# Performance work log

Hardware: AMD Instinct MI355X
Metric: run time of the kernel (lower is better)

## Reference

```python
import jax, jax.numpy as jnp
import numpy as np

N_NODES = 50000
N_EDGES = 800000
N_GRAPHS = 64
IN_DIM = 128
HID = 64      # per-head channels of conv1
HEADS1 = 4
OUT_DIM = 128
NEG_SLOPE = 0.2


def setup_inputs() -> dict:
    key = jax.random.key(0)
    ks = jax.random.split(key, 12)
    x = jax.random.normal(ks[0], (N_NODES, IN_DIM), dtype=jnp.float32)
    src = jax.random.randint(ks[1], (N_EDGES,), 0, N_NODES, dtype=jnp.int32)
    dst = jax.random.randint(ks[2], (N_EDGES,), 0, N_NODES, dtype=jnp.int32)
    batch = jnp.sort(jax.random.randint(ks[3], (N_NODES,), 0, N_GRAPHS, dtype=jnp.int32))
    s = 0.1
    W1 = jax.random.normal(ks[4], (IN_DIM, HEADS1 * HID), dtype=jnp.float32) * s
    a_src1 = jax.random.normal(ks[5], (HEADS1, HID), dtype=jnp.float32) * s
    a_dst1 = jax.random.normal(ks[6], (HEADS1, HID), dtype=jnp.float32) * s
    b1 = jnp.zeros((HEADS1 * HID,), dtype=jnp.float32)
    W2 = jax.random.normal(ks[7], (HEADS1 * HID, OUT_DIM), dtype=jnp.float32) * s
    a_src2 = jax.random.normal(ks[8], (1, OUT_DIM), dtype=jnp.float32) * s
    a_dst2 = jax.random.normal(ks[9], (1, OUT_DIM), dtype=jnp.float32) * s
    b2 = jnp.zeros((OUT_DIM,), dtype=jnp.float32)
    return {"x": x, "src": src, "dst": dst, "batch": batch,
            "W1": W1, "a_src1": a_src1, "a_dst1": a_dst1, "b1": b1,
            "W2": W2, "a_src2": a_src2, "a_dst2": a_dst2, "b2": b2}


def gat_conv(x, src, dst, W, a_src, a_dst, b, heads, ch, concat):
    """PyG-style GATConv (self-loops already appended to src/dst)."""
    n = x.shape[0]
    h = (x @ W).reshape(n, heads, ch)                     # [N,H,C]
    al_s = jnp.einsum('nhc,hc->nh', h, a_src)             # per-node src score
    al_d = jnp.einsum('nhc,hc->nh', h, a_dst)             # per-node dst score
    e = jax.nn.leaky_relu(al_s[src] + al_d[dst], NEG_SLOPE)  # [E,H]
    # segment softmax over incoming edges of each dst node
    m = jax.ops.segment_max(e, dst, num_segments=n)
    ex = jnp.exp(e - m[dst])
    den = jax.ops.segment_sum(ex, dst, num_segments=n)
    alpha = ex / den[dst]                                 # [E,H]
    out = jax.ops.segment_sum(alpha[:, :, None] * h[src], dst, num_segments=n)  # [N,H,C]
    out = out.reshape(n, heads * ch) if concat else out.mean(axis=1)
    return out + b


def reference(x, src, dst, batch, W1, a_src1, a_dst1, b1, W2, a_src2, a_dst2, b2):
    n = x.shape[0]
    loop = jnp.arange(n, dtype=src.dtype)
    s = jnp.concatenate([src, loop])   # add_self_loops=True (PyG default)
    d = jnp.concatenate([dst, loop])
    h = jax.nn.relu(gat_conv(x, s, d, W1, a_src1, a_dst1, b1, HEADS1, HID, True))
    h = gat_conv(h, s, d, W2, a_src2, a_dst2, b2, 1, OUT_DIM, False)
    # global_mean_pool over graph ids
    sums = jax.ops.segment_sum(h, batch, num_segments=N_GRAPHS)
    cnts = jax.ops.segment_sum(jnp.ones((n,), h.dtype), batch, num_segments=N_GRAPHS)
    return sums / jnp.maximum(cnts, 1.0)[:, None]
```

## Files before the change

kernel.cpp:

```cpp
#include <hip/hip_runtime.h>
#include <math.h>

#define NN 50000
#define NE 800000
#define ETOT (NE + NN)
#define NG 64
#define IND 128
#define HID1 64
#define H1HEADS 4
#define D1 256
#define D2 128
#define NEG 0.2f
#define CAP 64

typedef __attribute__((ext_vector_type(8))) short bf16x8;
typedef __attribute__((ext_vector_type(4))) float f32x4;

__device__ __forceinline__ unsigned short bf16rne(float f) {
    unsigned u = __float_as_uint(f);
    u = (u + 0x7FFFu + ((u >> 16) & 1u)) >> 16;
    return (unsigned short)u;
}
__device__ __forceinline__ float bf2f(unsigned short u) {
    return __uint_as_float(((unsigned)u) << 16);
}
__device__ __forceinline__ bf16x8 pack8(float4 a, float4 b) {
    bf16x8 r;
    r[0] = (short)bf16rne(a.x); r[1] = (short)bf16rne(a.y);
    r[2] = (short)bf16rne(a.z); r[3] = (short)bf16rne(a.w);
    r[4] = (short)bf16rne(b.x); r[5] = (short)bf16rne(b.y);
    r[6] = (short)bf16rne(b.z); r[7] = (short)bf16rne(b.w);
    return r;
}

__global__ __launch_bounds__(256) void build_fill(
        const int* __restrict__ src, const int* __restrict__ dst,
        const float* __restrict__ W1, unsigned short* __restrict__ W1t,
        const float* __restrict__ W2, unsigned short* __restrict__ W2t,
        const int* __restrict__ batch,
        int* __restrict__ deg, int* __restrict__ csrF,
        int* __restrict__ gstart) {
    const long E0 = ETOT;
    const long E1 = E0 + (long)IND * D1;
    const long E2 = E1 + (long)D1 * D2;
    const long T  = E2 + NG + 1;
    long i = (long)blockIdx.x * 256 + threadIdx.x;
    if (i >= T) return;
    if (i < E0) {
        int s = (i < NE) ? src[i] : (int)(i - NE);
        int d = (i < NE) ? dst[i] : (int)(i - NE);
        int slot = atomicAdd(&deg[d], 1);
        if (slot < CAP) csrF[d * CAP + slot] = s;
    } else if (i < E1) {
        int j = (int)(i - E0);
        int c_ = j / IND, r_ = j % IND;
        W1t[j] = bf16rne(W1[(long)r_ * D1 + c_]);
    } else if (i < E2) {
        int j = (int)(i - E1);
        int c_ = j / D1, r_ = j % D1;
        W2t[j] = bf16rne(W2[(long)r_ * D2 + c_]);
    } else {
        int g = (int)(i - E2);
        if (g == NG) gstart[NG] = NN;
        else {
            int lo = 0, hi = NN;
            while (lo < hi) {
                int mid = (lo + hi) >> 1;
                if (batch[mid] < g) lo = mid + 1; else hi = mid;
            }
            gstart[g] = lo;
        }
    }
}

template<int K, int N, int H, int AF32>
__global__ __launch_bounds__(256) void mfma_gemm_sc(int M,
                                                    const void* __restrict__ Ap,
                                                    const unsigned short* __restrict__ Bt,
                                                    const float* __restrict__ a_s,
                                                    const float* __restrict__ a_d,
                                                    unsigned short* __restrict__ C,
                                                    float* __restrict__ al_s,
                                                    float* __restrict__ al_d) {
    constexpr int NT = N / 16;
    constexpr int FPH = NT / H;
    const int w = threadIdx.x >> 6, l = threadIdx.x & 63;
    const int brow = blockIdx.x * 128 + w * 32;
    const int lr = l & 15, lk = (l >> 4) * 8;
    const int ar0 = min(brow + lr, M - 1);
    const int ar1 = min(brow + 16 + lr, M - 1);
    f32x4 acc[2][NT] = {};
    #pragma unroll
    for (int k0 = 0; k0 < K; k0 += 32) {
        bf16x8 af0, af1;
        if constexpr (AF32) {
            const float* a0 = (const float*)Ap + (long)ar0 * K + lk + k0;
            const float* a1 = (const float*)Ap + (long)ar1 * K + lk + k0;
            af0 = pack8(*reinterpret_cast<const float4*>(a0),
                        *reinterpret_cast<const float4*>(a0 + 4));
            af1 = pack8(*reinterpret_cast<const float4*>(a1),
                        *reinterpret_cast<const float4*>(a1 + 4));
        } else {
            af0 = *reinterpret_cast<const bf16x8*>((const unsigned short*)Ap + (long)ar0 * K + lk + k0);
            af1 = *reinterpret_cast<const bf16x8*>((const unsigned short*)Ap + (long)ar1 * K + lk + k0);
        }
        #pragma unroll
        for (int n = 0; n < NT; ++n) {
            bf16x8 bv = *reinterpret_cast<const bf16x8*>(Bt + (long)(n * 16 + lr) * K + lk + k0);
            acc[0][n] = __builtin_amdgcn_mfma_f32_16x16x32_bf16(af0, bv, acc[0][n], 0, 0, 0);
            acc[1][n] = __builtin_amdgcn_mfma_f32_16x16x32_bf16(af1, bv, acc[1][n], 0, 0, 0);
        }
    }
    float asv[NT], adv[NT];
    #pragma unroll
    for (int n = 0; n < NT; ++n) { asv[n] = a_s[n * 16 + lr]; adv[n] = a_d[n * 16 + lr]; }
    #pragma unroll
    for (int g = 0; g < 2; ++g) {
        const int orow = brow + g * 16 + (l >> 4) * 4;
        #pragma unroll
        for (int j = 0; j < 4; ++j) {
            int r = orow + j;
            bool ok = r < M;
            #pragma unroll
            for (int n = 0; n < NT; ++n)
                if (ok) C[(long)r * N + n * 16 + lr] = bf16rne(acc[g][n][j]);
            #pragma unroll
            for (int h = 0; h < H; ++h) {
                float ss = 0.f, sd = 0.f;
                #pragma unroll
                for (int f = 0; f < FPH; ++f) {
                    int n = h * FPH + f;
                    ss += acc[g][n][j] * asv[n];
                    sd += acc[g][n][j] * adv[n];
                }
                #pragma unroll
                for (int o = 8; o > 0; o >>= 1) {
                    ss += __shfl_xor(ss, o);
                    sd += __shfl_xor(sd, o);
                }
                if (ok && lr == 0) {
                    al_s[(long)r * H + h] = ss;
                    al_d[(long)r * H + h] = sd;
                }
            }
        }
    }
}

template<int H, int C, int RELU, int OUTBF>
__global__ __launch_bounds__(256) void gat_gather(const int* __restrict__ deg,
                                                  const int* __restrict__ csrF,
                                                  const float* __restrict__ als,
                                                  const float* __restrict__ ald,
                                                  const unsigned short* __restrict__ Hb,
                                                  const float* __restrict__ bias,
                                                  void* __restrict__ outp_) {
    constexpr int D = H * C;
    constexpr int VPL = D / 64;
    constexpr int HP = (H == 4) ? 5 : 1;
    __shared__ float sW[4][64][HP];
    __shared__ int   sS[4][64];
    const int lane = threadIdx.x & 63;
    const int w = threadIdx.x >> 6;
    const int n = blockIdx.x * 4 + w;
    if (n >= NN) return;
    const int h = (lane * VPL) / C;

    float aldv[H];
    #pragma unroll
    for (int hh = 0; hh < H; ++hh) aldv[hh] = ald[(long)n * H + hh];

    float acc[VPL] = {};
    float den = 0.f;

    const int cnt = min(deg[n], CAP);
    const bool valid = lane < cnt;
    const int s_l = valid ? csrF[n * CAP + lane] : 0;
    if constexpr (H == 4) {
        float4 a4 = *reinterpret_cast<const float4*>(als + (long)s_l * 4);
        float xs[4] = {a4.x, a4.y, a4.z, a4.w};
        #pragma unroll
        for (int hh = 0; hh < 4; ++hh) {
            float x = xs[hh] + aldv[hh];
            x = (x >= 0.f) ? x : NEG * x;
            sW[w][lane][hh] = valid ? __expf(x) : 0.f;
        }
    } else {
        float x = als[s_l] + aldv[0];
        x = (x >= 0.f) ? x : NEG * x;
        sW[w][lane][0] = valid ? __expf(x) : 0.f;
    }
    sS[w][lane] = s_l;

    int j0 = 0;
    for (; j0 + 8 <= cnt; j0 += 8) {
        int se[8]; float we[8];
        #pragma unroll
        for (int t = 0; t < 8; ++t) {
            se[t] = sS[w][j0 + t];
            we[t] = sW[w][j0 + t][h];
        }
        #pragma unroll
        for (int t = 0; t < 8; ++t) den += we[t];
        if constexpr (VPL == 4) {
            ushort4 aa[8];
            #pragma unroll
            for (int t = 0; t < 8; ++t)
                aa[t] = *reinterpret_cast<const ushort4*>(Hb + (long)se[t] * D + lane * 4);
            #pragma unroll
            for (int t = 0; t < 8; ++t) {
                acc[0] += we[t] * bf2f(aa[t].x); acc[1] += we[t] * bf2f(aa[t].y);
                acc[2] += we[t] * bf2f(aa[t].z); acc[3] += we[t] * bf2f(aa[t].w);
            }
        } else {
            ushort2 aa[8];
            #pragma unroll
            for (int t = 0; t < 8; ++t)
                aa[t] = *reinterpret_cast<const ushort2*>(Hb + (long)se[t] * D + lane * 2);
            #pragma unroll
            for (int t = 0; t < 8; ++t) {
                acc[0] += we[t] * bf2f(aa[t].x); acc[1] += we[t] * bf2f(aa[t].y);
            }
        }
    }
    for (; j0 < cnt; j0 += 4) {
        int se[4]; float we[4];
        #pragma unroll
        for (int t = 0; t < 4; ++t) {
            se[t] = sS[w][j0 + t];
            we[t] = sW[w][j0 + t][h];
        }
        #pragma unroll
        for (int t = 0; t < 4; ++t) den += we[t];
        if constexpr (VPL == 4) {
            ushort4 aa[4];
            #pragma unroll
            for (int t = 0; t < 4; ++t)
                aa[t] = *reinterpret_cast<const ushort4*>(Hb + (long)se[t] * D + lane * 4);
            #pragma unroll
            for (int t = 0; t < 4; ++t) {
                acc[0] += we[t] * bf2f(aa[t].x); acc[1] += we[t] * bf2f(aa[t].y);
                acc[2] += we[t] * bf2f(aa[t].z); acc[3] += we[t] * bf2f(aa[t].w);
            }
        } else {
            ushort2 aa[4];
            #pragma unroll
            for (int t = 0; t < 4; ++t)
                aa[t] = *reinterpret_cast<const ushort2*>(Hb + (long)se[t] * D + lane * 2);
            #pragma unroll
            for (int t = 0; t < 4; ++t) {
                acc[0] += we[t] * bf2f(aa[t].x); acc[1] += we[t] * bf2f(aa[t].y);
            }
        }
    }

    float inv = 1.f / den;
    float v[VPL];
    #pragma unroll
    for (int k = 0; k < VPL; ++k) {
        v[k] = acc[k] * inv + bias[lane * VPL + k];
        if (RELU) v[k] = fmaxf(v[k], 0.f);
    }
    if constexpr (OUTBF) {
        unsigned short* o = (unsigned short*)outp_;
        if constexpr (VPL == 4) {
            ushort4 p; p.x = bf16rne(v[0]); p.y = bf16rne(v[1]);
            p.z = bf16rne(v[2]); p.w = bf16rne(v[3]);
            *reinterpret_cast<ushort4*>(o + (long)n * D + lane * 4) = p;
        } else {
            ushort2 p; p.x = bf16rne(v[0]); p.y = bf16rne(v[1]);
            *reinterpret_cast<ushort2*>(o + (long)n * D + lane * 2) = p;
        }
    } else {
        float* o = (float*)outp_;
        if constexpr (VPL == 4) {
            float4 p = {v[0], v[1], v[2], v[3]};
            *reinterpret_cast<float4*>(o + (long)n * D + lane * 4) = p;
        } else {
            float2 p = {v[0], v[1]};
            *reinterpret_cast<float2*>(o + (long)n * D + lane * 2) = p;
        }
    }
}

__global__ __launch_bounds__(256) void pool_graph(const unsigned short* __restrict__ out2b,
                                                  const int* __restrict__ gstart,
                                                  float* __restrict__ out) {
    __shared__ float2 part[4][64];
    const int g = blockIdx.x;
    const int ch2 = threadIdx.x & 63;
    const int q = threadIdx.x >> 6;
    const int s = gstart[g], e = gstart[g + 1];
    float2 acc = {0.f, 0.f};
    for (int r = s + q; r < e; r += 4) {
        ushort2 v = *reinterpret_cast<const ushort2*>(out2b + (long)r * D2 + ch2 * 2);
        acc.x += bf2f(v.x);
        acc.y += bf2f(v.y);
    }
    part[q][ch2] = acc;
    __syncthreads();
    if (q == 0) {
        float inv = 1.f / fmaxf((float)(e - s), 1.f);
        float2 v;
        v.x = (part[0][ch2].x + part[1][ch2].x + part[2][ch2].x + part[3][ch2].x) * inv;
        v.y = (part[0][ch2].y + part[1][ch2].y + part[2][ch2].y + part[3][ch2].y) * inv;
        *reinterpret_cast<float2*>(out + g * D2 + ch2 * 2) = v;
    }
}

extern "C" void kernel_launch(void* const* d_in, const int* in_sizes, int n_in,
                              void* d_out, int out_size, void* d_ws, size_t ws_size,
                              hipStream_t stream) {
    const float* x      = (const float*)d_in[0];
    const int*   src    = (const int*)d_in[1];
    const int*   dst    = (const int*)d_in[2];
    const int*   batch  = (const int*)d_in[3];
    const float* W1     = (const float*)d_in[4];
    const float* a_src1 = (const float*)d_in[5];
    const float* a_dst1 = (const float*)d_in[6];
    const float* b1     = (const float*)d_in[7];
    const float* W2     = (const float*)d_in[8];
    const float* a_src2 = (const float*)d_in[9];
    const float* a_dst2 = (const float*)d_in[10];
    const float* b2     = (const float*)d_in[11];
    float* out = (float*)d_out;

    float* ws   = (float*)d_ws;
    float* als1 = ws;
    float* ald1 = als1 + (long)NN * H1HEADS;
    float* als2 = als1;
    float* ald2 = als1 + NN;
    unsigned short* Hb1   = (unsigned short*)(ald1 + (long)NN * H1HEADS);
    unsigned short* out1b = Hb1 + (long)NN * D1;
    unsigned short* Hb2   = out1b + (long)NN * D1;
    unsigned short* out2b = Hb2 + (long)NN * D2;
    unsigned short* W1t   = out2b + (long)NN * D2;
    unsigned short* W2t   = W1t + D1 * IND;
    int* deg    = (int*)(W2t + D2 * D1);
    int* csrF   = deg + NN;
    int* gstart = csrF + (long)NN * CAP;

    (void)hipMemsetAsync(deg, 0, NN * sizeof(int), stream);
    {
        long total = (long)ETOT + IND * D1 + D1 * D2 + NG + 1;
        build_fill<<<(int)((total + 255) / 256), 256, 0, stream>>>(
            src, dst, W1, W1t, W2, W2t, batch, deg, csrF, gstart);
    }

    mfma_gemm_sc<IND, D1, H1HEADS, 1><<<(NN + 127) / 128, 256, 0, stream>>>(
        NN, x, W1t, a_src1, a_dst1, Hb1, als1, ald1);
    gat_gather<H1HEADS, HID1, 1, 1><<<(NN + 3) / 4, 256, 0, stream>>>(
        deg, csrF, als1, ald1, Hb1, b1, out1b);

    mfma_gemm_sc<D1, D2, 1, 0><<<(NN + 127) / 128, 256, 0, stream>>>(
        NN, out1b, W2t, a_src2, a_dst2, Hb2, als2, ald2);
    gat_gather<1, D2, 0, 1><<<(NN + 3) / 4, 256, 0, stream>>>(
        deg, csrF, als2, ald2, Hb2, b2, out2b);

    pool_graph<<<NG, 256, 0, stream>>>(out2b, gstart, out);
}
```

Before: 272.6 us.

## Split layer-1 gather into two half-feature passes over column halves

The layer-1 gather, which handled all 256 features per node in one wave, is split into two launches. Each launch handles 128 columns, i.e. two heads. Each pass touches only half of every source row, so the working set of the random gathers is smaller and more likely to stay in cache. In exchange, the CSR lists and attention scores are read twice, the weights are recomputed, and there is an extra launch. The layer-2 gather is specialised into its own non-template kernel with equivalent logic.

```diff
diff --git a/kernel.cpp b/kernel.cpp
--- a/kernel.cpp
+++ b/kernel.cpp
@@ -147,50 +147,41 @@
     }
 }
 
-template<int H, int C, int RELU, int OUTBF>
-__global__ __launch_bounds__(256) void gat_gather(const int* __restrict__ deg,
-                                                  const int* __restrict__ csrF,
-                                                  const float* __restrict__ als,
-                                                  const float* __restrict__ ald,
-                                                  const unsigned short* __restrict__ Hb,
-                                                  const float* __restrict__ bias,
-                                                  void* __restrict__ outp_) {
-    constexpr int D = H * C;
-    constexpr int VPL = D / 64;
-    constexpr int HP = (H == 4) ? 5 : 1;
-    __shared__ float sW[4][64][HP];
+template<int P>
+__global__ __launch_bounds__(256) void gather1_half(const int* __restrict__ deg,
+                                                    const int* __restrict__ csrF,
+                                                    const float* __restrict__ als,
+                                                    const float* __restrict__ ald,
+                                                    const unsigned short* __restrict__ Hb,
+                                                    const float* __restrict__ bias,
+                                                    unsigned short* __restrict__ outp) {
+    __shared__ float sW[4][64][2];
     __shared__ int   sS[4][64];
     const int lane = threadIdx.x & 63;
     const int w = threadIdx.x >> 6;
     const int n = blockIdx.x * 4 + w;
     if (n >= NN) return;
-    const int h = (lane * VPL) / C;
-
-    float aldv[H];
-    #pragma unroll
-    for (int hh = 0; hh < H; ++hh) aldv[hh] = ald[(long)n * H + hh];
-
-    float acc[VPL] = {};
-    float den = 0.f;
+    const int hl = lane >> 5;
+    const int c0 = P * 128 + lane * 2;
+
+    float ald0 = ald[(long)n * 4 + P * 2 + 0];
+    float ald1 = ald[(long)n * 4 + P * 2 + 1];
+
+    float acc0 = 0.f, acc1 = 0.f, den = 0.f;
 
     const int cnt = min(deg[n], CAP);
     const bool valid = lane < cnt;
     const int s_l = valid ? csrF[n * CAP + lane] : 0;
-    if constexpr (H == 4) {
-        float4 a4 = *reinterpret_cast<const float4*>(als + (long)s_l * 4);
-        float xs[4] = {a4.x, a4.y, a4.z, a4.w};
-        #pragma unroll
-        for (int hh = 0; hh < 4; ++hh) {
-            float x = xs[hh] + aldv[hh];
-            x = (x >= 0.f) ? x : NEG * x;
-            sW[w][lane][hh] = valid ? __expf(x) : 0.f;
-        }
-    } else {
-        float x = als[s_l] + aldv[0];
-        x = (x >= 0.f) ? x : NEG * x;
-        sW[w][lane][0] = valid ? __expf(x) : 0.f;
-    }
-    sS[w][lane] = s_l;
+    {
+        float2 a2 = *reinterpret_cast<const float2*>(als + (long)s_l * 4 + P * 2);
+        float x0 = a2.x + ald0;
+        float x1 = a2.y + ald1;
+        x0 = (x0 >= 0.f) ? x0 : NEG * x0;
+        x1 = (x1 >= 0.f) ? x1 : NEG * x1;
+        sW[w][lane][0] = valid ? __expf(x0) : 0.f;
+        sW[w][lane][1] = valid ? __expf(x1) : 0.f;
+        sS[w][lane] = s_l;
+    }
 
     int j0 = 0;
     for (; j0 + 8 <= cnt; j0 += 8) {
@@ -198,29 +189,18 @@
         #pragma unroll
         for (int t = 0; t < 8; ++t) {
             se[t] = sS[w][j0 + t];
-            we[t] = sW[w][j0 + t][h];
+            we[t] = sW[w][j0 + t][hl];
         }
         #pragma unroll
         for (int t = 0; t < 8; ++t) den += we[t];
-        if constexpr (VPL == 4) {
-            ushort4 aa[8];
-            #pragma unroll
-            for (int t = 0; t < 8; ++t)
-                aa[t] = *reinterpret_cast<const ushort4*>(Hb + (long)se[t] * D + lane * 4);
-            #pragma unroll
-            for (int t = 0; t < 8; ++t) {
-                acc[0] += we[t] * bf2f(aa[t].x); acc[1] += we[t] * bf2f(aa[t].y);
-                acc[2] += we[t] * bf2f(aa[t].z); acc[3] += we[t] * bf2f(aa[t].w);
-            }
-        } else {
-            ushort2 aa[8];
-            #pragma unroll
-            for (int t = 0; t < 8; ++t)
-                aa[t] = *reinterpret_cast<const ushort2*>(Hb + (long)se[t] * D + lane * 2);
-            #pragma unroll
-            for (int t = 0; t < 8; ++t) {
-                acc[0] += we[t] * bf2f(aa[t].x); acc[1] += we[t] * bf2f(aa[t].y);
-            }
+        ushort2 aa[8];
+        #pragma unroll
+        for (int t = 0; t < 8; ++t)
+            aa[t] = *reinterpret_cast<const ushort2*>(Hb + (long)se[t] * D1 + c0);
+        #pragma unroll
+        for (int t = 0; t < 8; ++t) {
+            acc0 += we[t] * bf2f(aa[t].x);
+            acc1 += we[t] * bf2f(aa[t].y);
         }
     }
     for (; j0 < cnt; j0 += 4) {
@@ -228,59 +208,100 @@
         #pragma unroll
         for (int t = 0; t < 4; ++t) {
             se[t] = sS[w][j0 + t];
-            we[t] = sW[w][j0 + t][h];
+            we[t] = sW[w][j0 + t][hl];
         }
         #pragma unroll
         for (int t = 0; t < 4; ++t) den += we[t];
-        if constexpr (VPL == 4) {
-            ushort4 aa[4];
-            #pragma unroll
-            for (int t = 0; t < 4; ++t)
-                aa[t] = *reinterpret_cast<const ushort4*>(Hb + (long)se[t] * D + lane * 4);
-            #pragma unroll
-            for (int t = 0; t < 4; ++t) {
-                acc[0] += we[t] * bf2f(aa[t].x); acc[1] += we[t] * bf2f(aa[t].y);
-                acc[2] += we[t] * bf2f(aa[t].z); acc[3] += we[t] * bf2f(aa[t].w);
-            }
-        } else {
-            ushort2 aa[4];
-            #pragma unroll
-            for (int t = 0; t < 4; ++t)
-                aa[t] = *reinterpret_cast<const ushort2*>(Hb + (long)se[t] * D + lane * 2);
-            #pragma unroll
-            for (int t = 0; t < 4; ++t) {
-                acc[0] += we[t] * bf2f(aa[t].x); acc[1] += we[t] * bf2f(aa[t].y);
-            }
+        ushort2 aa[4];
+        #pragma unroll
+        for (int t = 0; t < 4; ++t)
+            aa[t] = *reinterpret_cast<const ushort2*>(Hb + (long)se[t] * D1 + c0);
+        #pragma unroll
+        for (int t = 0; t < 4; ++t) {
+            acc0 += we[t] * bf2f(aa[t].x);
+            acc1 += we[t] * bf2f(aa[t].y);
         }
     }
 
     float inv = 1.f / den;
-    float v[VPL];
-    #pragma unroll
-    for (int k = 0; k < VPL; ++k) {
-        v[k] = acc[k] * inv + bias[lane * VPL + k];
-        if (RELU) v[k] = fmaxf(v[k], 0.f);
-    }
-    if constexpr (OUTBF) {
-        unsigned short* o = (unsigned short*)outp_;
-        if constexpr (VPL == 4) {
-            ushort4 p; p.x = bf16rne(v[0]); p.y = bf16rne(v[1]);
-            p.z = bf16rne(v[2]); p.w = bf16rne(v[3]);
-            *reinterpret_cast<ushort4*>(o + (long)n * D + lane * 4) = p;
-        } else {
-            ushort2 p; p.x = bf16rne(v[0]); p.y = bf16rne(v[1]);
-            *reinterpret_cast<ushort2*>(o + (long)n * D + lane * 2) = p;
-        }
-    } else {
-        float* o = (float*)outp_;
-        if constexpr (VPL == 4) {
-            float4 p = {v[0], v[1], v[2], v[3]};
-            *reinterpret_cast<float4*>(o + (long)n * D + lane * 4) = p;
-        } else {
-            float2 p = {v[0], v[1]};
-            *reinterpret_cast<float2*>(o + (long)n * D + lane * 2) = p;
-        }
-    }
+    float v0 = fmaxf(acc0 * inv + bias[c0 + 0], 0.f);
+    float v1 = fmaxf(acc1 * inv + bias[c0 + 1], 0.f);
+    ushort2 p; p.x = bf16rne(v0); p.y = bf16rne(v1);
+    *reinterpret_cast<ushort2*>(outp + (long)n * D1 + c0) = p;
+}
+
+__global__ __launch_bounds__(256) void gat_gather2(const int* __restrict__ deg,
+                                                   const int* __restrict__ csrF,
+                                                   const float* __restrict__ als,
+                                                   const float* __restrict__ ald,
+                                                   const unsigned short* __restrict__ Hb,
+                                                   const float* __restrict__ bias,
+                                                   unsigned short* __restrict__ outp) {
+    __shared__ float sW[4][64];
+    __shared__ int   sS[4][64];
+    const int lane = threadIdx.x & 63;
+    const int w = threadIdx.x >> 6;
+    const int n = blockIdx.x * 4 + w;
+    if (n >= NN) return;
+
+    float aldv = ald[n];
+    float acc0 = 0.f, acc1 = 0.f, den = 0.f;
+
+    const int cnt = min(deg[n], CAP);
+    const bool valid = lane < cnt;
+    const int s_l = valid ? csrF[n * CAP + lane] : 0;
+    {
+        float x = als[s_l] + aldv;
+        x = (x >= 0.f) ? x : NEG * x;
+        sW[w][lane] = valid ? __expf(x) : 0.f;
+        sS[w][lane] = s_l;
+    }
+
+    int j0 = 0;
+    for (; j0 + 8 <= cnt; j0 += 8) {
+        int se[8]; float we[8];
+        #pragma unroll
+        for (int t = 0; t < 8; ++t) {
+            se[t] = sS[w][j0 + t];
+            we[t] = sW[w][j0 + t];
+        }
+        #pragma unroll
+        for (int t = 0; t < 8; ++t) den += we[t];
+        ushort2 aa[8];
+        #pragma unroll
+        for (int t = 0; t < 8; ++t)
+            aa[t] = *reinterpret_cast<const ushort2*>(Hb + (long)se[t] * D2 + lane * 2);
+        #pragma unroll
+        for (int t = 0; t < 8; ++t) {
+            acc0 += we[t] * bf2f(aa[t].x);
+            acc1 += we[t] * bf2f(aa[t].y);
+        }
+    }
+    for (; j0 < cnt; j0 += 4) {
+        int se[4]; float we[4];
+        #pragma unroll
+        for (int t = 0; t < 4; ++t) {
+            se[t] = sS[w][j0 + t];
+            we[t] = sW[w][j0 + t];
+        }
+        #pragma unroll
+        for (int t = 0; t < 4; ++t) den += we[t];
+        ushort2 aa[4];
+        #pragma unroll
+        for (int t = 0; t < 4; ++t)
+            aa[t] = *reinterpret_cast<const ushort2*>(Hb + (long)se[t] * D2 + lane * 2);
+        #pragma unroll
+        for (int t = 0; t < 4; ++t) {
+            acc0 += we[t] * bf2f(aa[t].x);
+            acc1 += we[t] * bf2f(aa[t].y);
+        }
+    }
+
+    float inv = 1.f / den;
+    float v0 = acc0 * inv + bias[lane * 2 + 0];
+    float v1 = acc1 * inv + bias[lane * 2 + 1];
+    ushort2 p; p.x = bf16rne(v0); p.y = bf16rne(v1);
+    *reinterpret_cast<ushort2*>(outp + (long)n * D2 + lane * 2) = p;
 }
 
 __global__ __launch_bounds__(256) void pool_graph(const unsigned short* __restrict__ out2b,
@@ -349,12 +370,14 @@
 
     mfma_gemm_sc<IND, D1, H1HEADS, 1><<<(NN + 127) / 128, 256, 0, stream>>>(
         NN, x, W1t, a_src1, a_dst1, Hb1, als1, ald1);
-    gat_gather<H1HEADS, HID1, 1, 1><<<(NN + 3) / 4, 256, 0, stream>>>(
+    gather1_half<0><<<(NN + 3) / 4, 256, 0, stream>>>(
+        deg, csrF, als1, ald1, Hb1, b1, out1b);
+    gather1_half<1><<<(NN + 3) / 4, 256, 0, stream>>>(
         deg, csrF, als1, ald1, Hb1, b1, out1b);
 
     mfma_gemm_sc<D1, D2, 1, 0><<<(NN + 127) / 128, 256, 0, stream>>>(
         NN, out1b, W2t, a_src2, a_dst2, Hb2, als2, ald2);
-    gat_gather<1, D2, 0, 1><<<(NN + 3) / 4, 256, 0, stream>>>(
+    gat_gather2<<<(NN + 3) / 4, 256, 0, stream>>>(
         deg, csrF, als2, ald2, Hb2, b2, out2b);
 
     pool_graph<<<NG, 256, 0, stream>>>(out2b, gstart, out);
```

After: 271.6 us. No clear change (-0.4%).

## Fuse edge scatter into first GEMM launch and fold degree zeroing into prep

Applied to the files above, without the earlier changes.

The hipMemset of the degree array is removed and the zeroing moves into a prep kernel that also converts the weights and computes graph starts. The edge-bucketing atomics now run as extra blocks in the same launch as the first MFMA GEMM, so the atomic-bound scatter and the compute-bound GEMM can overlap on the GPU and two launches are saved. The gather epilogue now writes bf16 element by element instead of as packed vector stores, which may cost some store efficiency.

```diff
diff --git a/kernel.cpp b/kernel.cpp
--- a/kernel.cpp
+++ b/kernel.cpp
@@ -12,6 +12,8 @@
 #define D2 128
 #define NEG 0.2f
 #define CAP 64
+#define G1B ((NN + 127) / 128)
+#define SCB ((ETOT + 255) / 256)
 
 typedef __attribute__((ext_vector_type(8))) short bf16x8;
 typedef __attribute__((ext_vector_type(4))) float f32x4;
@@ -33,34 +35,30 @@
     return r;
 }
 
-__global__ __launch_bounds__(256) void build_fill(
-        const int* __restrict__ src, const int* __restrict__ dst,
-        const float* __restrict__ W1, unsigned short* __restrict__ W1t,
-        const float* __restrict__ W2, unsigned short* __restrict__ W2t,
-        const int* __restrict__ batch,
-        int* __restrict__ deg, int* __restrict__ csrF,
-        int* __restrict__ gstart) {
-    const long E0 = ETOT;
-    const long E1 = E0 + (long)IND * D1;
-    const long E2 = E1 + (long)D1 * D2;
-    const long T  = E2 + NG + 1;
-    long i = (long)blockIdx.x * 256 + threadIdx.x;
+__global__ __launch_bounds__(256) void prep(const float* __restrict__ W1,
+                                            unsigned short* __restrict__ W1t,
+                                            const float* __restrict__ W2,
+                                            unsigned short* __restrict__ W2t,
+                                            const int* __restrict__ batch,
+                                            int* __restrict__ deg,
+                                            int* __restrict__ gstart) {
+    const int E1 = IND * D1;
+    const int E2 = E1 + D1 * D2;
+    const int E3 = E2 + NN;
+    const int T  = E3 + NG + 1;
+    int i = blockIdx.x * 256 + threadIdx.x;
     if (i >= T) return;
-    if (i < E0) {
-        int s = (i < NE) ? src[i] : (int)(i - NE);
-        int d = (i < NE) ? dst[i] : (int)(i - NE);
-        int slot = atomicAdd(&deg[d], 1);
-        if (slot < CAP) csrF[d * CAP + slot] = s;
-    } else if (i < E1) {
-        int j = (int)(i - E0);
-        int c_ = j / IND, r_ = j % IND;
-        W1t[j] = bf16rne(W1[(long)r_ * D1 + c_]);
+    if (i < E1) {
+        int c_ = i / IND, r_ = i % IND;
+        W1t[i] = bf16rne(W1[(long)r_ * D1 + c_]);
     } else if (i < E2) {
-        int j = (int)(i - E1);
+        int j = i - E1;
         int c_ = j / D1, r_ = j % D1;
         W2t[j] = bf16rne(W2[(long)r_ * D2 + c_]);
+    } else if (i < E3) {
+        deg[i - E2] = 0;
     } else {
-        int g = (int)(i - E2);
+        int g = i - E3;
         if (g == NG) gstart[NG] = NN;
         else {
             int lo = 0, hi = NN;
@@ -73,9 +71,86 @@
     }
 }
 
-template<int K, int N, int H, int AF32>
+__global__ __launch_bounds__(256) void gemm1_scatter(
+        const float* __restrict__ x, const unsigned short* __restrict__ W1t,
+        const float* __restrict__ a_s, const float* __restrict__ a_d,
+        unsigned short* __restrict__ C,
+        float* __restrict__ al_s, float* __restrict__ al_d,
+        const int* __restrict__ src, const int* __restrict__ dst,
+        int* __restrict__ deg, int* __restrict__ csrF) {
+    if (blockIdx.x >= G1B) {
+        long i = (long)(blockIdx.x - G1B) * 256 + threadIdx.x;
+        if (i < ETOT) {
+            int s = (i < NE) ? src[i] : (int)(i - NE);
+            int d = (i < NE) ? dst[i] : (int)(i - NE);
+            int slot = atomicAdd(&deg[d], 1);
+            if (slot < CAP) csrF[d * CAP + slot] = s;
+        }
+        return;
+    }
+    constexpr int K = IND, N = D1, H = H1HEADS;
+    constexpr int NT = N / 16;
+    constexpr int FPH = NT / H;
+    const int w = threadIdx.x >> 6, l = threadIdx.x & 63;
+    const int brow = blockIdx.x * 128 + w * 32;
+    const int lr = l & 15, lk = (l >> 4) * 8;
+    const int ar0 = min(brow + lr, NN - 1);
+    const int ar1 = min(brow + 16 + lr, NN - 1);
+    f32x4 acc[2][NT] = {};
+    #pragma unroll
+    for (int k0 = 0; k0 < K; k0 += 32) {
+        const float* a0 = x + (long)ar0 * K + lk + k0;
+        const float* a1 = x + (long)ar1 * K + lk + k0;
+        bf16x8 af0 = pack8(*reinterpret_cast<const float4*>(a0),
+                           *reinterpret_cast<const float4*>(a0 + 4));
+        bf16x8 af1 = pack8(*reinterpret_cast<const float4*>(a1),
+                           *reinterpret_cast<const float4*>(a1 + 4));
+        #pragma unroll
+        for (int n = 0; n < NT; ++n) {
+            bf16x8 bv = *reinterpret_cast<const bf16x8*>(W1t + (long)(n * 16 + lr) * K + lk + k0);
+            acc[0][n] = __builtin_amdgcn_mfma_f32_16x16x32_bf16(af0, bv, acc[0][n], 0, 0, 0);
+            acc[1][n] = __builtin_amdgcn_mfma_f32_16x16x32_bf16(af1, bv, acc[1][n], 0, 0, 0);
+        }
+    }
+    float asv[NT], adv[NT];
+    #pragma unroll
+    for (int n = 0; n < NT; ++n) { asv[n] = a_s[n * 16 + lr]; adv[n] = a_d[n * 16 + lr]; }
+    #pragma unroll
+    for (int g = 0; g < 2; ++g) {
+        const int orow = brow + g * 16 + (l >> 4) * 4;
+        #pragma unroll
+        for (int j = 0; j < 4; ++j) {
+            int r = orow + j;
+            bool ok = r < NN;
+            #pragma unroll
+            for (int n = 0; n < NT; ++n)
+                if (ok) C[(long)r * N + n * 16 + lr] = bf16rne(acc[g][n][j]);
+            #pragma unroll
+            for (int h = 0; h < H; ++h) {
+                float ss = 0.f, sd = 0.f;
+                #pragma unroll
+                for (int f = 0; f < FPH; ++f) {
+                    int n = h * FPH + f;
+                    ss += acc[g][n][j] * asv[n];
+                    sd += acc[g][n][j] * adv[n];
+                }
+                #pragma unroll
+                for (int o = 8; o > 0; o >>= 1) {
+                    ss += __shfl_xor(ss, o);
+                    sd += __shfl_xor(sd, o);
+                }
+                if (ok && lr == 0) {
+                    al_s[(long)r * H + h] = ss;
+                    al_d[(long)r * H + h] = sd;
+                }
+            }
+        }
+    }
+}
+
+template<int K, int N, int H>
 __global__ __launch_bounds__(256) void mfma_gemm_sc(int M,
-                                                    const void* __restrict__ Ap,
+                                                    const unsigned short* __restrict__ A,
                                                     const unsigned short* __restrict__ Bt,
                                                     const float* __restrict__ a_s,
                                                     const float* __restrict__ a_d,
@@ -92,18 +167,8 @@
     f32x4 acc[2][NT] = {};
     #pragma unroll
     for (int k0 = 0; k0 < K; k0 += 32) {
-        bf16x8 af0, af1;
-        if constexpr (AF32) {
-            const float* a0 = (const float*)Ap + (long)ar0 * K + lk + k0;
-            const float* a1 = (const float*)Ap + (long)ar1 * K + lk + k0;
-            af0 = pack8(*reinterpret_cast<const float4*>(a0),
-                        *reinterpret_cast<const float4*>(a0 + 4));
-            af1 = pack8(*reinterpret_cast<const float4*>(a1),
-                        *reinterpret_cast<const float4*>(a1 + 4));
-        } else {
-            af0 = *reinterpret_cast<const bf16x8*>((const unsigned short*)Ap + (long)ar0 * K + lk + k0);
-            af1 = *reinterpret_cast<const bf16x8*>((const unsigned short*)Ap + (long)ar1 * K + lk + k0);
-        }
+        bf16x8 af0 = *reinterpret_cast<const bf16x8*>(A + (long)ar0 * K + lk + k0);
+        bf16x8 af1 = *reinterpret_cast<const bf16x8*>(A + (long)ar1 * K + lk + k0);
         #pragma unroll
         for (int n = 0; n < NT; ++n) {
             bf16x8 bv = *reinterpret_cast<const bf16x8*>(Bt + (long)(n * 16 + lr) * K + lk + k0);
@@ -147,14 +212,14 @@
     }
 }
 
-template<int H, int C, int RELU, int OUTBF>
+template<int H, int C, int RELU>
 __global__ __launch_bounds__(256) void gat_gather(const int* __restrict__ deg,
                                                   const int* __restrict__ csrF,
                                                   const float* __restrict__ als,
                                                   const float* __restrict__ ald,
                                                   const unsigned short* __restrict__ Hb,
                                                   const float* __restrict__ bias,
-                                                  void* __restrict__ outp_) {
+                                                  unsigned short* __restrict__ outp) {
     constexpr int D = H * C;
     constexpr int VPL = D / 64;
     constexpr int HP = (H == 4) ? 5 : 1;
@@ -255,31 +320,11 @@
     }
 
     float inv = 1.f / den;
-    float v[VPL];
     #pragma unroll
     for (int k = 0; k < VPL; ++k) {
-        v[k] = acc[k] * inv + bias[lane * VPL + k];
-        if (RELU) v[k] = fmaxf(v[k], 0.f);
-    }
-    if constexpr (OUTBF) {
-        unsigned short* o = (unsigned short*)outp_;
-        if constexpr (VPL == 4) {
-            ushort4 p; p.x = bf16rne(v[0]); p.y = bf16rne(v[1]);
-            p.z = bf16rne(v[2]); p.w = bf16rne(v[3]);
-            *reinterpret_cast<ushort4*>(o + (long)n * D + lane * 4) = p;
-        } else {
-            ushort2 p; p.x = bf16rne(v[0]); p.y = bf16rne(v[1]);
-            *reinterpret_cast<ushort2*>(o + (long)n * D + lane * 2) = p;
-        }
-    } else {
-        float* o = (float*)outp_;
-        if constexpr (VPL == 4) {
-            float4 p = {v[0], v[1], v[2], v[3]};
-            *reinterpret_cast<float4*>(o + (long)n * D + lane * 4) = p;
-        } else {
-            float2 p = {v[0], v[1]};
-            *reinterpret_cast<float2*>(o + (long)n * D + lane * 2) = p;
-        }
+        float v = acc[k] * inv + bias[lane * VPL + k];
+        if (RELU) v = fmaxf(v, 0.f);
+        outp[(long)n * D + lane * VPL + k] = bf16rne(v);
     }
 }
 
@@ -340,21 +385,20 @@
     int* csrF   = deg + NN;
     int* gstart = csrF + (long)NN * CAP;
 
-    (void)hipMemsetAsync(deg, 0, NN * sizeof(int), stream);
     {
-        long total = (long)ETOT + IND * D1 + D1 * D2 + NG + 1;
-        build_fill<<<(int)((total + 255) / 256), 256, 0, stream>>>(
-            src, dst, W1, W1t, W2, W2t, batch, deg, csrF, gstart);
-    }
-
-    mfma_gemm_sc<IND, D1, H1HEADS, 1><<<(NN + 127) / 128, 256, 0, stream>>>(
-        NN, x, W1t, a_src1, a_dst1, Hb1, als1, ald1);
-    gat_gather<H1HEADS, HID1, 1, 1><<<(NN + 3) / 4, 256, 0, stream>>>(
+        int total = IND * D1 + D1 * D2 + NN + NG + 1;
+        prep<<<(total + 255) / 256, 256, 0, stream>>>(W1, W1t, W2, W2t, batch, deg, gstart);
+    }
+
+    gemm1_scatter<<<G1B + SCB, 256, 0, stream>>>(
+        x, W1t, a_src1, a_dst1, Hb1, als1, ald1, src, dst, deg, csrF);
+
+    gat_gather<H1HEADS, HID1, 1><<<(NN + 3) / 4, 256, 0, stream>>>(
         deg, csrF, als1, ald1, Hb1, b1, out1b);
 
-    mfma_gemm_sc<D1, D2, 1, 0><<<(NN + 127) / 128, 256, 0, stream>>>(
+    mfma_gemm_sc<D1, D2, 1><<<(NN + 127) / 128, 256, 0, stream>>>(
         NN, out1b, W2t, a_src2, a_dst2, Hb2, als2, ald2);
-    gat_gather<1, D2, 0, 1><<<(NN + 3) / 4, 256, 0, stream>>>(
+    gat_gather<1, D2, 0><<<(NN + 3) / 4, 256, 0, stream>>>(
         deg, csrF, als2, ald2, Hb2, b2, out2b);
 
     pool_graph<<<NG, 256, 0, stream>>>(out2b, gstart, out);
```

Result: faster. 244.0 us (median of 2 runs) (-10.5%).
